# Kernel tuning notes

Hardware: AMD Instinct MI355X
Metric: run time of the kernel (lower is better)

## Reference

```python
import jax, jax.numpy as jnp
import numpy as np

NUM_HEADS = 2
LN_EPS = 1e-5


def layer_norm(x, w, b):
    mu = jnp.mean(x, axis=-1, keepdims=True)
    var = jnp.mean(jnp.square(x - mu), axis=-1, keepdims=True)
    return (x - mu) * jax.lax.rsqrt(var + LN_EPS) * w + b


def setup_inputs() -> dict:
    key = jax.random.key(0)
    ks = jax.random.split(key, 8)
    B, N, C = 8, 2048, 1024
    H = 2 * C  # mlp hidden
    s = lambda fan_in: 1.0 / np.sqrt(fan_in)
    return {
        "x": jax.random.normal(ks[0], (B, N, C), dtype=jnp.float32),
        "ln1_w": jnp.ones((C,), jnp.float32),
        "ln1_b": jnp.zeros((C,), jnp.float32),
        "qkv_w": jax.random.normal(ks[1], (C, 3 * C), jnp.float32) * s(C),
        "qkv_b": jnp.zeros((3 * C,), jnp.float32),
        "proj_w": jax.random.normal(ks[2], (C, C), jnp.float32) * s(C),
        "proj_b": jnp.zeros((C,), jnp.float32),
        "ln2_w": jnp.ones((C,), jnp.float32),
        "ln2_b": jnp.zeros((C,), jnp.float32),
        "mlp_w1": jax.random.normal(ks[3], (C, H), jnp.float32) * s(C),
        "mlp_b1": jnp.zeros((H,), jnp.float32),
        "mlp_w2": jax.random.normal(ks[4], (H, C), jnp.float32) * s(H),
        "mlp_b2": jnp.zeros((C,), jnp.float32),
    }


def reference(x, ln1_w, ln1_b, qkv_w, qkv_b, proj_w, proj_b, ln2_w, ln2_b,
              mlp_w1, mlp_b1, mlp_w2, mlp_b2):
    B, N, C = x.shape
    h = NUM_HEADS
    d = C // h
    scale = d ** -0.5

    # --- attention branch ---
    xn = layer_norm(x, ln1_w, ln1_b)
    qkv = (xn @ qkv_w + qkv_b).reshape(B, N, 3, h, d)
    q, k, v = jnp.moveaxis(qkv, 2, 0)          # each [B, N, h, d]
    q = jnp.swapaxes(q, 1, 2)                  # [B, h, N, d]
    k = jnp.swapaxes(k, 1, 2)
    v = jnp.swapaxes(v, 1, 2)
    attn = jnp.einsum("bhnd,bhmd->bhnm", q, k) * scale
    attn = jax.nn.softmax(attn, axis=-1)       # [B, h, N, N]
    out = jnp.einsum("bhnm,bhmd->bhnd", attn, v)
    out = jnp.swapaxes(out, 1, 2).reshape(B, N, C)
    out = out @ proj_w + proj_b
    x = x + out

    # --- mlp branch ---
    xn = layer_norm(x, ln2_w, ln2_b)
    hdn = jax.nn.gelu(xn @ mlp_w1 + mlp_b1, approximate=False)
    x = x + (hdn @ mlp_w2 + mlp_b2)
    return x
```

## Files before the change

### kernel.cpp

```cpp
#include <hip/hip_runtime.h>
#include <hip/hip_bf16.h>
#include <math.h>

#define TILE 128
#define BK 32

using short8  = __attribute__((ext_vector_type(8))) short;
using short4v = __attribute__((ext_vector_type(4))) short;
using f32x4   = __attribute__((ext_vector_type(4))) float;
typedef __hip_bfloat16 bf16;

constexpr int BB = 8, SEQ = 2048, C = 1024, H3 = 3072, DH = 512, MH = 2048;
constexpr int MR = BB * SEQ;

enum {
  F_TRANSB = 1,
  F_GELU   = 2,
  F_RES    = 4,
  F_OUTBF16= 8,
  F_BIAS   = 16,
  F_SCALE  = 32,
  F_RESF32 = 64
};

struct ZOffs { long long a[16]; long long b[16]; long long c[16]; };

__device__ __forceinline__ float bf2f(bf16 h) { return __bfloat162float(h); }

__device__ __forceinline__ void gload16(const void* g, void* l) {
  __builtin_amdgcn_global_load_lds(
      (const __attribute__((address_space(1))) unsigned int*)g,
      (__attribute__((address_space(3))) unsigned int*)l, 16, 0, 0);
}

template<int FLAGS>
__global__ __launch_bounds__(256) void gemm_k(
    const bf16* __restrict__ A,
    const bf16* __restrict__ B,
    void* __restrict__ Dst,
    const float* __restrict__ bias,
    const void* __restrict__ res,
    int K, int lda, int ldb, int ldc,
    float scale, ZOffs zo)
{
  __shared__ __align__(16) unsigned short As[TILE * BK];
  __shared__ __align__(16) unsigned short Bs[TILE * BK];
  const int tid = threadIdx.x;
  const int z = blockIdx.z;
  const int m0 = blockIdx.y * TILE, n0 = blockIdx.x * TILE;
  const bf16* Ab = A + zo.a[z];
  const bf16* Bb = B + zo.b[z];
  const long long coff = zo.c[z];
  const int wave = tid >> 6, lane = tid & 63;
  const int wm = (wave & 1) << 6, wn = (wave >> 1) << 6;
  const int lr = lane & 15, lq = lane >> 4;

  int srow[2], skb[2];
  #pragma unroll
  for (int i = 0; i < 2; i++) {
    int c = tid + (i << 8);
    srow[i] = c >> 2;
    skb[i]  = (c & 3) ^ ((srow[i] >> 1) & 3);
  }
  const bf16* Asrc[2]; const bf16* Bsrc[2] = {nullptr, nullptr};
  #pragma unroll
  for (int i = 0; i < 2; i++)
    Asrc[i] = Ab + (size_t)(m0 + srow[i]) * lda + skb[i] * 8;
  if (FLAGS & F_TRANSB) {
    #pragma unroll
    for (int i = 0; i < 2; i++)
      Bsrc[i] = Bb + (size_t)(n0 + srow[i]) * ldb + skb[i] * 8;
  }

  f32x4 acc[4][4] = {};
  const int swl = (lr >> 1) & 3;

  for (int k0 = 0; k0 < K; k0 += BK) {
    #pragma unroll
    for (int i = 0; i < 2; i++)
      gload16(Asrc[i] + k0, &As[(tid + (i << 8)) * 8]);
    if (FLAGS & F_TRANSB) {
      #pragma unroll
      for (int i = 0; i < 2; i++)
        gload16(Bsrc[i] + k0, &Bs[(tid + (i << 8)) * 8]);
    } else {
      #pragma unroll
      for (int i = 0; i < 2; i++) {
        int c = tid + (i << 8);
        int kk = c >> 4, nn = (c & 15) << 3;
        unsigned short tmp[8];
        *(uint4*)tmp = *(const uint4*)(Bb + (size_t)(k0 + kk) * ldb + n0 + nn);
        #pragma unroll
        for (int j = 0; j < 8; j++) {
          int n = nn + j;
          Bs[n * BK + (((kk >> 3) ^ ((n >> 1) & 3)) << 3) + (kk & 7)] = tmp[j];
        }
      }
    }
    __syncthreads();
    short8 af[4], bfr[4];
    #pragma unroll
    for (int mi = 0; mi < 4; mi++)
      af[mi] = *(const short8*)&As[(wm + mi * 16 + lr) * BK + ((lq ^ swl) << 3)];
    #pragma unroll
    for (int ni = 0; ni < 4; ni++)
      bfr[ni] = *(const short8*)&Bs[(wn + ni * 16 + lr) * BK + ((lq ^ swl) << 3)];
    #pragma unroll
    for (int mi = 0; mi < 4; mi++)
      #pragma unroll
      for (int ni = 0; ni < 4; ni++)
        acc[mi][ni] = __builtin_amdgcn_mfma_f32_16x16x32_bf16(
            af[mi], bfr[ni], acc[mi][ni], 0, 0, 0);
    __syncthreads();
  }

  #pragma unroll
  for (int mi = 0; mi < 4; mi++) {
    #pragma unroll
    for (int ni = 0; ni < 4; ni++) {
      int col = n0 + wn + ni * 16 + lr;
      float bv = (FLAGS & F_BIAS) ? bias[col] : 0.0f;
      #pragma unroll
      for (int r = 0; r < 4; r++) {
        int row = m0 + wm + mi * 16 + lq * 4 + r;
        float v = acc[mi][ni][r];
        if (FLAGS & F_SCALE) v *= scale;
        v += bv;
        if (FLAGS & F_GELU) v = 0.5f * v * (1.0f + erff(v * 0.70710678118654752f));
        if (FLAGS & F_RES) {
          size_t ridx = (size_t)row * ldc + col;
          v += (FLAGS & F_RESF32) ? ((const float*)res)[ridx]
                                  : bf2f(((const bf16*)res)[ridx]);
        }
        size_t idx = (size_t)coff + (size_t)row * ldc + col;
        if (FLAGS & F_OUTBF16) ((bf16*)Dst)[idx] = __float2bfloat16(v);
        else                   ((float*)Dst)[idx] = v;
      }
    }
  }
}

template<int FLAGS>
__global__ __launch_bounds__(512, 2) void gemm256_k(
    const bf16* __restrict__ A,
    const bf16* __restrict__ B,
    void* __restrict__ Dst,
    const float* __restrict__ bias,
    const void* __restrict__ res,
    int K, int lda, int ldb, int ldc,
    float scale, ZOffs zo)
{
  static_assert(FLAGS & F_TRANSB, "gemm256_k requires B^T layout");
  extern __shared__ __align__(16) unsigned short smem[];
  unsigned short* AsAll = smem;
  unsigned short* BsAll = smem + 4 * 256 * 32;

  const int tid = threadIdx.x;
  const int z = blockIdx.z;
  const int m0 = blockIdx.y * 256, n0 = blockIdx.x * 256;
  const bf16* Ab = A + zo.a[z];
  const bf16* Bb = B + zo.b[z];
  const long long coff = zo.c[z];
  const int wave = tid >> 6, lane = tid & 63;
  const int wm = wave >> 2, wn = wave & 3;
  const int lr = lane & 15, lq = lane >> 4;
  const int swl = (lr >> 1) & 3;
  const int kcol = (lq ^ swl) << 3;

  const bf16* Asrc[2]; const bf16* Bsrc[2];
  #pragma unroll
  for (int i = 0; i < 2; i++) {
    int c = tid + (i << 9);
    int row = c >> 2;
    int ks  = (c & 3) ^ ((row >> 1) & 3);
    Asrc[i] = Ab + (size_t)(m0 + row) * lda + ks * 8;
    Bsrc[i] = Bb + (size_t)(n0 + row) * ldb + ks * 8;
  }
  const int d0 = tid * 8, d1 = (tid + 512) * 8;

  const int nt = K >> 5;

  const int npro = nt < 3 ? nt : 3;
  for (int t = 0; t < npro; ++t) {
    unsigned short* At_ = AsAll + (t & 3) * 8192;
    unsigned short* Bt_ = BsAll + (t & 3) * 8192;
    const int k0 = t * 32;
    gload16(Asrc[0] + k0, At_ + d0);
    gload16(Asrc[1] + k0, At_ + d1);
    gload16(Bsrc[0] + k0, Bt_ + d0);
    gload16(Bsrc[1] + k0, Bt_ + d1);
  }

  f32x4 acc[8][4] = {};
  short8 af[4], bfr[2];

#define RD_A(mh_)                                                            \
  _Pragma("unroll")                                                          \
  for (int m_ = 0; m_ < 4; ++m_)                                             \
    af[m_] = *(const short8*)&At[(wm * 128 + (mh_) * 64 + m_ * 16 + lr) * 32 + kcol];

#define RD_B(nh_)                                                            \
  _Pragma("unroll")                                                          \
  for (int n_ = 0; n_ < 2; ++n_)                                             \
    bfr[n_] = *(const short8*)&Bt[(wn * 64 + (nh_) * 32 + n_ * 16 + lr) * 32 + kcol];

#define MM(mh_, nh_)                                                         \
  __builtin_amdgcn_s_setprio(1);                                             \
  _Pragma("unroll")                                                          \
  for (int m_ = 0; m_ < 4; ++m_)                                             \
    _Pragma("unroll")                                                        \
    for (int n_ = 0; n_ < 2; ++n_)                                           \
      acc[(mh_) * 4 + m_][(nh_) * 2 + n_] =                                  \
          __builtin_amdgcn_mfma_f32_16x16x32_bf16(                           \
              af[m_], bfr[n_], acc[(mh_) * 4 + m_][(nh_) * 2 + n_], 0, 0, 0);\
  __builtin_amdgcn_s_setprio(0);

  for (int t = 0; t < nt; ++t) {
    const int ahead = nt - 1 - t;
    if (ahead >= 2)      asm volatile("s_waitcnt vmcnt(8)" ::: "memory");
    else if (ahead == 1) asm volatile("s_waitcnt vmcnt(4)" ::: "memory");
    else                 asm volatile("s_waitcnt vmcnt(0)" ::: "memory");
    __builtin_amdgcn_s_barrier();

    const unsigned short* At = AsAll + (t & 3) * 8192;
    const unsigned short* Bt = BsAll + (t & 3) * 8192;
    const int ts = t + 3;
    const bool st = ts < nt;
    unsigned short* Ad = AsAll + (ts & 3) * 8192;
    unsigned short* Bd = BsAll + (ts & 3) * 8192;
    const int ks0 = ts * 32;

    RD_A(0); RD_B(0);
    if (st) gload16(Asrc[0] + ks0, Ad + d0);
    __builtin_amdgcn_s_barrier();
    MM(0, 0);
    __builtin_amdgcn_s_barrier();

    RD_B(1);
    if (st) gload16(Asrc[1] + ks0, Ad + d1);
    __builtin_amdgcn_s_barrier();
    MM(0, 1);
    __builtin_amdgcn_s_barrier();

    RD_A(1);
    if (st) gload16(Bsrc[0] + ks0, Bd + d0);
    __builtin_amdgcn_s_barrier();
    MM(1, 1);
    __builtin_amdgcn_s_barrier();

    RD_B(0);
    if (st) gload16(Bsrc[1] + ks0, Bd + d1);
    __builtin_amdgcn_s_barrier();
    MM(1, 0);
    __builtin_amdgcn_s_barrier();
  }

#undef RD_A
#undef RD_B
#undef MM

  const int colBase = n0 + wn * 64 + lr;
  float bv[4];
  #pragma unroll
  for (int n = 0; n < 4; ++n)
    bv[n] = (FLAGS & F_BIAS) ? bias[colBase + n * 16] : 0.0f;
  #pragma unroll
  for (int m = 0; m < 8; ++m) {
    #pragma unroll
    for (int n = 0; n < 4; ++n) {
      const int col = colBase + n * 16;
      #pragma unroll
      for (int r = 0; r < 4; ++r) {
        const int row = m0 + wm * 128 + m * 16 + lq * 4 + r;
        float v = acc[m][n][r];
        if (FLAGS & F_SCALE) v *= scale;
        v += bv[n];
        if (FLAGS & F_GELU) v = 0.5f * v * (1.0f + erff(v * 0.70710678118654752f));
        if (FLAGS & F_RES) {
          size_t ridx = (size_t)row * ldc + col;
          v += (FLAGS & F_RESF32) ? ((const float*)res)[ridx]
                                  : bf2f(((const bf16*)res)[ridx]);
        }
        size_t idx = (size_t)coff + (size_t)row * ldc + col;
        if (FLAGS & F_OUTBF16) ((bf16*)Dst)[idx] = __float2bfloat16(v);
        else                   ((float*)Dst)[idx] = v;
      }
    }
  }
}

__global__ __launch_bounds__(256) void tconv_kernel(
    const float* __restrict__ src, bf16* __restrict__ dst, int K, int N)
{
  __shared__ float t[32][33];
  int n0 = blockIdx.x * 32, k0 = blockIdx.y * 32;
  int c = threadIdx.x & 31, r = threadIdx.x >> 5;
  #pragma unroll
  for (int i = 0; i < 4; i++)
    t[r + i * 8][c] = src[(size_t)(k0 + r + i * 8) * N + n0 + c];
  __syncthreads();
  #pragma unroll
  for (int i = 0; i < 4; i++)
    dst[(size_t)(n0 + r + i * 8) * K + k0 + c] = __float2bfloat16(t[c][r + i * 8]);
}

__global__ __launch_bounds__(256) void vtrans_kernel(
    const bf16* __restrict__ qkv, bf16* __restrict__ vt)
{
  __shared__ unsigned short t[32][33];
  int bh = blockIdx.z, b = bh >> 1, h = bh & 1;
  int n0 = blockIdx.x * 32, d0 = blockIdx.y * 32;
  int c = threadIdx.x & 31, r = threadIdx.x >> 5;
  const bf16* src = qkv + (size_t)b * SEQ * H3 + 2 * C + (size_t)h * DH;
  #pragma unroll
  for (int i = 0; i < 4; i++)
    t[r + i * 8][c] = *(const unsigned short*)&src[(size_t)(n0 + r + i * 8) * H3 + d0 + c];
  __syncthreads();
  bf16* dst = vt + ((size_t)bh * DH + d0) * SEQ + n0;
  #pragma unroll
  for (int i = 0; i < 4; i++)
    *(unsigned short*)&dst[(size_t)(r + i * 8) * SEQ + c] = t[c][r + i * 8];
}

__device__ __forceinline__ void ld4(const float* p, float v[4]) {
  const float4 t = *(const float4*)p;
  v[0] = t.x; v[1] = t.y; v[2] = t.z; v[3] = t.w;
}
__device__ __forceinline__ void ld4(const bf16* p, float v[4]) {
  short4v t = *(const short4v*)p;
  #pragma unroll
  for (int i = 0; i < 4; ++i) v[i] = bf2f(((const bf16*)&t)[i]);
}

template<typename T>
__global__ __launch_bounds__(256) void ln_kernel(
    const T* __restrict__ x,
    const float* __restrict__ w,
    const float* __restrict__ b,
    bf16* __restrict__ out)
{
  __shared__ float sm[4], sm2[4];
  int row = blockIdx.x, tid = threadIdx.x;
  float v[4];
  ld4(x + (size_t)row * 1024 + tid * 4, v);
  float s  = v[0] + v[1] + v[2] + v[3];
  float sq = v[0]*v[0] + v[1]*v[1] + v[2]*v[2] + v[3]*v[3];
  #pragma unroll
  for (int o = 32; o > 0; o >>= 1) {
    s  += __shfl_down(s, o, 64);
    sq += __shfl_down(sq, o, 64);
  }
  int wvi = tid >> 6, lnn = tid & 63;
  if (lnn == 0) { sm[wvi] = s; sm2[wvi] = sq; }
  __syncthreads();
  s  = sm[0] + sm[1] + sm[2] + sm[3];
  sq = sm2[0] + sm2[1] + sm2[2] + sm2[3];
  float mean = s * (1.0f / 1024.0f);
  float var  = sq * (1.0f / 1024.0f) - mean * mean;
  float rs = rsqrtf(var + 1e-5f);
  float wv4[4], bv4[4];
  ld4(w + tid * 4, wv4);
  ld4(b + tid * 4, bv4);
  short4v o4;
  #pragma unroll
  for (int i = 0; i < 4; ++i)
    ((bf16*)&o4)[i] = __float2bfloat16((v[i] - mean) * rs * wv4[i] + bv4[i]);
  *(short4v*)&out[(size_t)row * 1024 + tid * 4] = o4;
}

__global__ __launch_bounds__(256) void softmax_kernel(
    bf16* __restrict__ sc)
{
  __shared__ float sm[4];
  int tid = threadIdx.x;
  size_t base = ((size_t)blockIdx.y * 2048 + blockIdx.x) * 2048 + (size_t)tid * 8;
  short8 sv = *(const short8*)&sc[base];
  float v[8], m = -1e30f;
  #pragma unroll
  for (int i = 0; i < 8; i++) { v[i] = bf2f(((const bf16*)&sv)[i]); m = fmaxf(m, v[i]); }
  #pragma unroll
  for (int o = 32; o > 0; o >>= 1) m = fmaxf(m, __shfl_down(m, o, 64));
  int wvi = tid >> 6, lnn = tid & 63;
  if (lnn == 0) sm[wvi] = m;
  __syncthreads();
  m = fmaxf(fmaxf(sm[0], sm[1]), fmaxf(sm[2], sm[3]));
  __syncthreads();
  float s = 0.f;
  #pragma unroll
  for (int i = 0; i < 8; i++) { v[i] = __expf(v[i] - m); s += v[i]; }
  #pragma unroll
  for (int o = 32; o > 0; o >>= 1) s += __shfl_down(s, o, 64);
  if (lnn == 0) sm[wvi] = s;
  __syncthreads();
  s = sm[0] + sm[1] + sm[2] + sm[3];
  float inv = 1.0f / s;
  short8 ov;
  #pragma unroll
  for (int i = 0; i < 8; i++)
    ((bf16*)&ov)[i] = __float2bfloat16(v[i] * inv);
  *(short8*)&sc[base] = ov;
}

#define G256(FL, grid_, A_, B_, D_, bias_, res_, K_, lda_, ldb_, ldc_, sc_, zo_)      \
  do {                                                                                \
    (void)hipFuncSetAttribute(reinterpret_cast<const void*>(&gemm256_k<(FL)>),        \
                              hipFuncAttributeMaxDynamicSharedMemorySize, 131072);    \
    hipLaunchKernelGGL((gemm256_k<(FL)>), grid_, dim3(512), 131072, stream,           \
                       A_, B_, D_, bias_, res_, K_, lda_, ldb_, ldc_, sc_, zo_);      \
  } while (0)

extern "C" void kernel_launch(void* const* d_in, const int* in_sizes, int n_in,
                              void* d_out, int out_size, void* d_ws, size_t ws_size,
                              hipStream_t stream) {
  const float* x      = (const float*)d_in[0];
  const float* ln1_w  = (const float*)d_in[1];
  const float* ln1_b  = (const float*)d_in[2];
  const float* qkv_w  = (const float*)d_in[3];
  const float* qkv_b  = (const float*)d_in[4];
  const float* proj_w = (const float*)d_in[5];
  const float* proj_b = (const float*)d_in[6];
  const float* ln2_w  = (const float*)d_in[7];
  const float* ln2_b  = (const float*)d_in[8];
  const float* mlp_w1 = (const float*)d_in[9];
  const float* mlp_b1 = (const float*)d_in[10];
  const float* mlp_w2 = (const float*)d_in[11];
  const float* mlp_b2 = (const float*)d_in[12];
  float* out = (float*)d_out;

  char* ws = (char*)d_ws;
  const size_t MB = 1ull << 20;
  bf16* qkvT  = (bf16*)ws;
  bf16* projT = qkvT + 3 * 1024 * 1024;
  bf16* w1T   = qkvT + 4 * 1024 * 1024;
  bf16* w2T   = qkvT + 6 * 1024 * 1024;
  bf16* xn    = (bf16*)(ws + 16 * MB);
  bf16* qkvb  = (bf16*)(ws + 48 * MB);
  bf16* h1    = qkvb;
  bf16* Vt    = (bf16*)(ws + 144 * MB);

  int CH; bool useVt, x1f32;
  if      (ws_size >= 304 * MB) { CH = 16; useVt = true;  x1f32 = true;  }
  else if (ws_size >= 240 * MB) { CH = 8;  useVt = true;  x1f32 = true;  }
  else if (ws_size >= 208 * MB) { CH = 4;  useVt = true;  x1f32 = false; }
  else                          { CH = 4;  useVt = false; x1f32 = false; }
  char* R = ws + (useVt ? 176 * MB : 144 * MB);
  bf16*  scores = (bf16*)R;
  float* x1f    = (float*)R;
  bf16*  x1h    = (bf16*)R;

  ZOffs z0 = {};
  const float scale = 0.04419417382415922f;
  dim3 blk(256);

  hipLaunchKernelGGL(tconv_kernel, dim3(H3 / 32, C / 32), blk, 0, stream, qkv_w, qkvT, C, H3);
  hipLaunchKernelGGL(tconv_kernel, dim3(C / 32, C / 32), blk, 0, stream, proj_w, projT, C, C);
  hipLaunchKernelGGL(tconv_kernel, dim3(MH / 32, C / 32), blk, 0, stream, mlp_w1, w1T, C, MH);
  hipLaunchKernelGGL(tconv_kernel, dim3(C / 32, MH / 32), blk, 0, stream, mlp_w2, w2T, MH, C);

  hipLaunchKernelGGL((ln_kernel<float>), dim3(MR), blk, 0, stream, x, ln1_w, ln1_b, xn);

  G256(F_TRANSB | F_BIAS | F_OUTBF16, dim3(H3 / 256, MR / 256, 1),
       xn, qkvT, (void*)qkvb, qkv_b, nullptr, C, C, C, H3, 1.0f, z0);

  if (useVt)
    hipLaunchKernelGGL(vtrans_kernel, dim3(SEQ / 32, DH / 32, 16), blk, 0, stream, qkvb, Vt);

  for (int ch = 0; ch < 16 / CH; ch++) {
    ZOffs zq = {}, zp = {};
    for (int zz = 0; zz < CH; zz++) {
      int bh = ch * CH + zz, b = bh >> 1, hh = bh & 1;
      zq.a[zz] = (long long)b * SEQ * H3 + (long long)hh * DH;
      zq.b[zz] = (long long)b * SEQ * H3 + C + (long long)hh * DH;
      zq.c[zz] = (long long)zz * SEQ * SEQ;
      zp.a[zz] = (long long)zz * SEQ * SEQ;
      zp.b[zz] = useVt ? (long long)bh * DH * SEQ
                       : (long long)b * SEQ * H3 + 2 * C + (long long)hh * DH;
      zp.c[zz] = (long long)b * SEQ * C + (long long)hh * DH;
    }
    G256(F_TRANSB | F_SCALE | F_OUTBF16, dim3(SEQ / 256, SEQ / 256, CH),
         qkvb, qkvb, (void*)scores, nullptr, nullptr, DH, H3, H3, SEQ, scale, zq);
    hipLaunchKernelGGL(softmax_kernel, dim3(SEQ, CH), blk, 0, stream, scores);
    if (useVt)
      G256(F_TRANSB | F_OUTBF16, dim3(DH / 256, SEQ / 256, CH),
           scores, Vt, (void*)xn, nullptr, nullptr, SEQ, SEQ, SEQ, C, 1.0f, zp);
    else
      hipLaunchKernelGGL((gemm_k<F_OUTBF16>),
                         dim3(DH / TILE, SEQ / TILE, CH), blk, 0, stream,
                         scores, qkvb, (void*)xn, nullptr, nullptr, SEQ, SEQ, H3, C, 1.0f, zp);
  }

  if (x1f32) {
    G256(F_TRANSB | F_BIAS | F_RES | F_RESF32, dim3(C / 256, MR / 256, 1),
         xn, projT, (void*)x1f, proj_b, (const void*)x, C, C, C, C, 1.0f, z0);
    hipLaunchKernelGGL((ln_kernel<float>), dim3(MR), blk, 0, stream, x1f, ln2_w, ln2_b, xn);
  } else {
    G256(F_TRANSB | F_BIAS | F_RES | F_RESF32 | F_OUTBF16, dim3(C / 256, MR / 256, 1),
         xn, projT, (void*)x1h, proj_b, (const void*)x, C, C, C, C, 1.0f, z0);
    hipLaunchKernelGGL((ln_kernel<bf16>), dim3(MR), blk, 0, stream, x1h, ln2_w, ln2_b, xn);
  }

  G256(F_TRANSB | F_BIAS | F_GELU | F_OUTBF16, dim3(MH / 256, MR / 256, 1),
       xn, w1T, (void*)h1, mlp_b1, nullptr, C, C, C, MH, 1.0f, z0);

  if (x1f32) {
    G256(F_TRANSB | F_BIAS | F_RES | F_RESF32, dim3(C / 256, MR / 256, 1),
         h1, w2T, (void*)out, mlp_b2, (const void*)x1f, MH, MH, MH, C, 1.0f, z0);
  } else {
    G256(F_TRANSB | F_BIAS | F_RES, dim3(C / 256, MR / 256, 1),
         h1, w2T, (void*)out, mlp_b2, (const void*)x1h, MH, MH, MH, C, 1.0f, z0);
  }
}
```

Measured before the change: 836.3 us.

## Restructure 256x256 GEMM to BK=64 double buffering with register-held B fragments

The 256-tile GEMM moves from a 4-stage BK=32 LDS ring to a 2-stage BK=64 double buffer with an 8-way XOR swizzle. Each wave keeps both halves of its B fragments in registers so the last MFMA quadrant needs no LDS read, which allows stores into the current buffer during compute and removes one barrier pair per k-step. It also remaps workgroup IDs in groups of eight to improve L2 locality. The cost is more VGPRs for fragments and a shallower prefetch depth in tiles, and the remap assumes the workgroup count divides evenly by eight.

```diff
diff --git a/kernel.cpp b/kernel.cpp
--- a/kernel.cpp
+++ b/kernel.cpp
@@ -152,111 +152,134 @@
 {
   static_assert(FLAGS & F_TRANSB, "gemm256_k requires B^T layout");
   extern __shared__ __align__(16) unsigned short smem[];
-  unsigned short* AsAll = smem;
-  unsigned short* BsAll = smem + 4 * 256 * 32;
 
   const int tid = threadIdx.x;
   const int z = blockIdx.z;
-  const int m0 = blockIdx.y * 256, n0 = blockIdx.x * 256;
+
+  const int gx = gridDim.x;
+  const int nwg = gx * gridDim.y;
+  const int wg = blockIdx.y * gx + blockIdx.x;
+  const int cpx = nwg >> 3;
+  const int swz = (wg & 7) * cpx + (wg >> 3);
+  const int m0 = (swz / gx) * 256, n0 = (swz % gx) * 256;
+
   const bf16* Ab = A + zo.a[z];
   const bf16* Bb = B + zo.b[z];
   const long long coff = zo.c[z];
   const int wave = tid >> 6, lane = tid & 63;
   const int wm = wave >> 2, wn = wave & 3;
   const int lr = lane & 15, lq = lane >> 4;
-  const int swl = (lr >> 1) & 3;
-  const int kcol = (lq ^ swl) << 3;
-
-  const bf16* Asrc[2]; const bf16* Bsrc[2];
-  #pragma unroll
-  for (int i = 0; i < 2; i++) {
-    int c = tid + (i << 9);
-    int row = c >> 2;
-    int ks  = (c & 3) ^ ((row >> 1) & 3);
-    Asrc[i] = Ab + (size_t)(m0 + row) * lda + ks * 8;
-    Bsrc[i] = Bb + (size_t)(n0 + row) * ldb + ks * 8;
-  }
-  const int d0 = tid * 8, d1 = (tid + 512) * 8;
-
-  const int nt = K >> 5;
-
-  const int npro = nt < 3 ? nt : 3;
-  for (int t = 0; t < npro; ++t) {
-    unsigned short* At_ = AsAll + (t & 3) * 8192;
-    unsigned short* Bt_ = BsAll + (t & 3) * 8192;
-    const int k0 = t * 32;
-    gload16(Asrc[0] + k0, At_ + d0);
-    gload16(Asrc[1] + k0, At_ + d1);
-    gload16(Bsrc[0] + k0, Bt_ + d0);
-    gload16(Bsrc[1] + k0, Bt_ + d1);
+  const int r7 = lr & 7;
+  const int sk0 = (lq ^ r7) << 3;
+  const int sk1 = ((4 + lq) ^ r7) << 3;
+  const int rowA = (wm * 128 + lr) * 64;
+  const int rowB = (wn * 64 + lr) * 64;
+
+  const int t8 = tid >> 3, s8 = tid & 7;
+  const int sslot = (s8 ^ (t8 & 7)) << 3;
+  const bf16* srcA = Ab + (size_t)(m0 + t8) * lda + sslot;
+  const int rB0 = (t8 & 31) + ((t8 >> 5) << 6);
+  const bf16* srcB = Bb + (size_t)(n0 + rB0) * ldb + sslot;
+  const int dA0 = tid * 8;
+  const int dB0 = rB0 * 64 + s8 * 8;
+
+  const int nt = K >> 6;
+
+#define SA(h_, ks_, Ad_)                                                       \
+  do {                                                                         \
+    gload16(srcA + (size_t)((h_) * 64) * lda + (ks_),                          \
+            (Ad_) + dA0 + (h_) * 4096);                                        \
+    gload16(srcA + (size_t)((h_) * 64 + 128) * lda + (ks_),                    \
+            (Ad_) + dA0 + (h_) * 4096 + 8192);                                 \
+  } while (0)
+#define SB(h_, ks_, Bd_)                                                       \
+  do {                                                                         \
+    gload16(srcB + (size_t)((h_) * 32) * ldb + (ks_),                          \
+            (Bd_) + dB0 + (h_) * 2048);                                        \
+    gload16(srcB + (size_t)((h_) * 32 + 128) * ldb + (ks_),                    \
+            (Bd_) + dB0 + (h_) * 2048 + 8192);                                 \
+  } while (0)
+
+  {
+    const int npro = nt < 2 ? nt : 2;
+    for (int t = 0; t < npro; ++t) {
+      unsigned short* Ad = smem + (t & 1) * 16384;
+      unsigned short* Bd = smem + 32768 + (t & 1) * 16384;
+      const int ks = t * 64;
+      SA(0, ks, Ad); SA(1, ks, Ad); SB(0, ks, Bd); SB(1, ks, Bd);
+    }
   }
 
   f32x4 acc[8][4] = {};
-  short8 af[4], bfr[2];
-
-#define RD_A(mh_)                                                            \
-  _Pragma("unroll")                                                          \
-  for (int m_ = 0; m_ < 4; ++m_)                                             \
-    af[m_] = *(const short8*)&At[(wm * 128 + (mh_) * 64 + m_ * 16 + lr) * 32 + kcol];
-
-#define RD_B(nh_)                                                            \
-  _Pragma("unroll")                                                          \
-  for (int n_ = 0; n_ < 2; ++n_)                                             \
-    bfr[n_] = *(const short8*)&Bt[(wn * 64 + (nh_) * 32 + n_ * 16 + lr) * 32 + kcol];
-
-#define MM(mh_, nh_)                                                         \
-  __builtin_amdgcn_s_setprio(1);                                             \
-  _Pragma("unroll")                                                          \
-  for (int m_ = 0; m_ < 4; ++m_)                                             \
-    _Pragma("unroll")                                                        \
-    for (int n_ = 0; n_ < 2; ++n_)                                           \
-      acc[(mh_) * 4 + m_][(nh_) * 2 + n_] =                                  \
-          __builtin_amdgcn_mfma_f32_16x16x32_bf16(                           \
-              af[m_], bfr[n_], acc[(mh_) * 4 + m_][(nh_) * 2 + n_], 0, 0, 0);\
+  short8 af0[4], af1[4];
+  short8 bA0[2], bA1[2];
+  short8 bB0[2], bB1[2];
+
+#define RD_AF(mh_)                                                             \
+  _Pragma("unroll")                                                            \
+  for (int m_ = 0; m_ < 4; ++m_) {                                             \
+    af0[m_] = *(const short8*)&At[rowA + ((mh_) * 64 + m_ * 16) * 64 + sk0];   \
+    af1[m_] = *(const short8*)&At[rowA + ((mh_) * 64 + m_ * 16) * 64 + sk1];   \
+  }
+#define RD_BF(nh_, b0_, b1_)                                                   \
+  _Pragma("unroll")                                                            \
+  for (int n_ = 0; n_ < 2; ++n_) {                                             \
+    b0_[n_] = *(const short8*)&Bt[rowB + ((nh_) * 32 + n_ * 16) * 64 + sk0];   \
+    b1_[n_] = *(const short8*)&Bt[rowB + ((nh_) * 32 + n_ * 16) * 64 + sk1];   \
+  }
+#define MM(mh_, nh_, b0_, b1_)                                                 \
+  __builtin_amdgcn_s_setprio(1);                                               \
+  _Pragma("unroll")                                                            \
+  for (int m_ = 0; m_ < 4; ++m_)                                               \
+    _Pragma("unroll")                                                          \
+    for (int n_ = 0; n_ < 2; ++n_) {                                           \
+      acc[(mh_) * 4 + m_][(nh_) * 2 + n_] =                                    \
+          __builtin_amdgcn_mfma_f32_16x16x32_bf16(                             \
+              af0[m_], b0_[n_], acc[(mh_) * 4 + m_][(nh_) * 2 + n_], 0, 0, 0); \
+      acc[(mh_) * 4 + m_][(nh_) * 2 + n_] =                                    \
+          __builtin_amdgcn_mfma_f32_16x16x32_bf16(                             \
+              af1[m_], b1_[n_], acc[(mh_) * 4 + m_][(nh_) * 2 + n_], 0, 0, 0); \
+    }                                                                          \
   __builtin_amdgcn_s_setprio(0);
 
   for (int t = 0; t < nt; ++t) {
-    const int ahead = nt - 1 - t;
-    if (ahead >= 2)      asm volatile("s_waitcnt vmcnt(8)" ::: "memory");
-    else if (ahead == 1) asm volatile("s_waitcnt vmcnt(4)" ::: "memory");
-    else                 asm volatile("s_waitcnt vmcnt(0)" ::: "memory");
-    __builtin_amdgcn_s_barrier();
-
-    const unsigned short* At = AsAll + (t & 3) * 8192;
-    const unsigned short* Bt = BsAll + (t & 3) * 8192;
-    const int ts = t + 3;
-    const bool st = ts < nt;
-    unsigned short* Ad = AsAll + (ts & 3) * 8192;
-    unsigned short* Bd = BsAll + (ts & 3) * 8192;
-    const int ks0 = ts * 32;
-
-    RD_A(0); RD_B(0);
-    if (st) gload16(Asrc[0] + ks0, Ad + d0);
-    __builtin_amdgcn_s_barrier();
-    MM(0, 0);
-    __builtin_amdgcn_s_barrier();
-
-    RD_B(1);
-    if (st) gload16(Asrc[1] + ks0, Ad + d1);
-    __builtin_amdgcn_s_barrier();
-    MM(0, 1);
-    __builtin_amdgcn_s_barrier();
-
-    RD_A(1);
-    if (st) gload16(Bsrc[0] + ks0, Bd + d0);
-    __builtin_amdgcn_s_barrier();
-    MM(1, 1);
-    __builtin_amdgcn_s_barrier();
-
-    RD_B(0);
-    if (st) gload16(Bsrc[1] + ks0, Bd + d1);
-    __builtin_amdgcn_s_barrier();
-    MM(1, 0);
-    __builtin_amdgcn_s_barrier();
-  }
-
-#undef RD_A
-#undef RD_B
+    if (t == nt - 1) asm volatile("s_waitcnt vmcnt(0)" ::: "memory");
+    else             asm volatile("s_waitcnt vmcnt(8)" ::: "memory");
+    __builtin_amdgcn_s_barrier();
+
+    const unsigned short* At = smem + (t & 1) * 16384;
+    const unsigned short* Bt = smem + 32768 + (t & 1) * 16384;
+    unsigned short* Ad = smem + (t & 1) * 16384;
+    unsigned short* Bd = smem + 32768 + (t & 1) * 16384;
+    const bool st = (t + 2) < nt;
+    const int ks = (t + 2) * 64;
+
+    RD_AF(0);
+    RD_BF(0, bA0, bA1);
+    __builtin_amdgcn_s_barrier();
+    MM(0, 0, bA0, bA1);
+    __builtin_amdgcn_s_barrier();
+
+    RD_BF(1, bB0, bB1);
+    if (st) { SA(0, ks, Ad); SB(0, ks, Bd); }
+    __builtin_amdgcn_s_barrier();
+    MM(0, 1, bB0, bB1);
+    __builtin_amdgcn_s_barrier();
+
+    RD_AF(1);
+    if (st) { SB(1, ks, Bd); }
+    __builtin_amdgcn_s_barrier();
+    MM(1, 1, bB0, bB1);
+    __builtin_amdgcn_s_barrier();
+
+    if (st) { SA(1, ks, Ad); }
+    MM(1, 0, bA0, bA1);
+  }
+
+#undef SA
+#undef SB
+#undef RD_AF
+#undef RD_BF
 #undef MM
 
   const int colBase = n0 + wn * 64 + lr;
```

Result: faster. 765.5 us (-8.5%).

## Restructure 256-tile GEMM into 3-stage pipeline with one barrier per K-step and XCD swizzle

Applied to the files above, without the earlier changes.

Replaces the 4-stage LDS ring, which interleaved loads, MFMA phases and eight barriers per K-step, with a 3-stage ring. Each K-step now waits once, issues the global-to-LDS load two steps ahead, and runs all 32 MFMAs after a single barrier. A and B tiles of each stage are packed contiguously, which cuts dynamic LDS from 128 KB to 96 KB. Block indices are also remapped so consecutive workgroups spread across the 8 XCDs in contiguous chunks, to improve L2 reuse. The goal is less barrier overhead and better cache locality, at the cost of one fewer stage of prefetch depth; the swizzle assumes the x*y grid size is divisible by 8.

```diff
diff --git a/kernel.cpp b/kernel.cpp
--- a/kernel.cpp
+++ b/kernel.cpp
@@ -152,12 +152,17 @@
 {
   static_assert(FLAGS & F_TRANSB, "gemm256_k requires B^T layout");
   extern __shared__ __align__(16) unsigned short smem[];
-  unsigned short* AsAll = smem;
-  unsigned short* BsAll = smem + 4 * 256 * 32;
 
   const int tid = threadIdx.x;
   const int z = blockIdx.z;
-  const int m0 = blockIdx.y * 256, n0 = blockIdx.x * 256;
+
+  const int gx = gridDim.x;
+  const int nwg = gx * gridDim.y;
+  const int wg = blockIdx.y * gx + blockIdx.x;
+  const int cpx = nwg >> 3;
+  const int swz = (wg & 7) * cpx + (wg >> 3);
+  const int m0 = (swz / gx) * 256, n0 = (swz % gx) * 256;
+
   const bf16* Ab = A + zo.a[z];
   const bf16* Bb = B + zo.b[z];
   const long long coff = zo.c[z];
@@ -167,97 +172,65 @@
   const int swl = (lr >> 1) & 3;
   const int kcol = (lq ^ swl) << 3;
 
-  const bf16* Asrc[2]; const bf16* Bsrc[2];
-  #pragma unroll
-  for (int i = 0; i < 2; i++) {
-    int c = tid + (i << 9);
-    int row = c >> 2;
-    int ks  = (c & 3) ^ ((row >> 1) & 3);
-    Asrc[i] = Ab + (size_t)(m0 + row) * lda + ks * 8;
-    Bsrc[i] = Bb + (size_t)(n0 + row) * ldb + ks * 8;
-  }
-  const int d0 = tid * 8, d1 = (tid + 512) * 8;
+  const int c0 = tid, c1 = tid + 512;
+  const int row0 = c0 >> 2, sl0 = (c0 & 3) ^ ((row0 >> 1) & 3);
+  const int row1 = c1 >> 2, sl1 = (c1 & 3) ^ ((row1 >> 1) & 3);
+  const bf16* sA0 = Ab + (size_t)(m0 + row0) * lda + sl0 * 8;
+  const bf16* sA1 = Ab + (size_t)(m0 + row1) * lda + sl1 * 8;
+  const bf16* sB0 = Bb + (size_t)(n0 + row0) * ldb + sl0 * 8;
+  const bf16* sB1 = Bb + (size_t)(n0 + row1) * ldb + sl1 * 8;
+  const int dst0 = c0 * 8, dst1 = c1 * 8;
 
   const int nt = K >> 5;
 
-  const int npro = nt < 3 ? nt : 3;
-  for (int t = 0; t < npro; ++t) {
-    unsigned short* At_ = AsAll + (t & 3) * 8192;
-    unsigned short* Bt_ = BsAll + (t & 3) * 8192;
-    const int k0 = t * 32;
-    gload16(Asrc[0] + k0, At_ + d0);
-    gload16(Asrc[1] + k0, At_ + d1);
-    gload16(Bsrc[0] + k0, Bt_ + d0);
-    gload16(Bsrc[1] + k0, Bt_ + d1);
-  }
+#define STAGE(ks_, D_)                                                         \
+  do {                                                                         \
+    gload16(sA0 + (ks_), (D_) + dst0);                                         \
+    gload16(sA1 + (ks_), (D_) + dst1);                                         \
+    gload16(sB0 + (ks_), (D_) + 8192 + dst0);                                  \
+    gload16(sB1 + (ks_), (D_) + 8192 + dst1);                                  \
+  } while (0)
+
+  STAGE(0, smem);
+  if (nt > 1) STAGE(32, smem + 16384);
 
   f32x4 acc[8][4] = {};
-  short8 af[4], bfr[2];
-
-#define RD_A(mh_)                                                            \
-  _Pragma("unroll")                                                          \
-  for (int m_ = 0; m_ < 4; ++m_)                                             \
-    af[m_] = *(const short8*)&At[(wm * 128 + (mh_) * 64 + m_ * 16 + lr) * 32 + kcol];
-
-#define RD_B(nh_)                                                            \
-  _Pragma("unroll")                                                          \
-  for (int n_ = 0; n_ < 2; ++n_)                                             \
-    bfr[n_] = *(const short8*)&Bt[(wn * 64 + (nh_) * 32 + n_ * 16 + lr) * 32 + kcol];
-
-#define MM(mh_, nh_)                                                         \
-  __builtin_amdgcn_s_setprio(1);                                             \
-  _Pragma("unroll")                                                          \
-  for (int m_ = 0; m_ < 4; ++m_)                                             \
-    _Pragma("unroll")                                                        \
-    for (int n_ = 0; n_ < 2; ++n_)                                           \
-      acc[(mh_) * 4 + m_][(nh_) * 2 + n_] =                                  \
-          __builtin_amdgcn_mfma_f32_16x16x32_bf16(                           \
-              af[m_], bfr[n_], acc[(mh_) * 4 + m_][(nh_) * 2 + n_], 0, 0, 0);\
-  __builtin_amdgcn_s_setprio(0);
+  short8 af[4], bf4[4];
+  int bc = 0, bs = 2;
 
   for (int t = 0; t < nt; ++t) {
-    const int ahead = nt - 1 - t;
-    if (ahead >= 2)      asm volatile("s_waitcnt vmcnt(8)" ::: "memory");
-    else if (ahead == 1) asm volatile("s_waitcnt vmcnt(4)" ::: "memory");
-    else                 asm volatile("s_waitcnt vmcnt(0)" ::: "memory");
+    if (t == nt - 1) asm volatile("s_waitcnt vmcnt(0)" ::: "memory");
+    else             asm volatile("s_waitcnt vmcnt(4)" ::: "memory");
     __builtin_amdgcn_s_barrier();
-
-    const unsigned short* At = AsAll + (t & 3) * 8192;
-    const unsigned short* Bt = BsAll + (t & 3) * 8192;
-    const int ts = t + 3;
-    const bool st = ts < nt;
-    unsigned short* Ad = AsAll + (ts & 3) * 8192;
-    unsigned short* Bd = BsAll + (ts & 3) * 8192;
-    const int ks0 = ts * 32;
-
-    RD_A(0); RD_B(0);
-    if (st) gload16(Asrc[0] + ks0, Ad + d0);
-    __builtin_amdgcn_s_barrier();
-    MM(0, 0);
-    __builtin_amdgcn_s_barrier();
-
-    RD_B(1);
-    if (st) gload16(Asrc[1] + ks0, Ad + d1);
-    __builtin_amdgcn_s_barrier();
-    MM(0, 1);
-    __builtin_amdgcn_s_barrier();
-
-    RD_A(1);
-    if (st) gload16(Bsrc[0] + ks0, Bd + d0);
-    __builtin_amdgcn_s_barrier();
-    MM(1, 1);
-    __builtin_amdgcn_s_barrier();
-
-    RD_B(0);
-    if (st) gload16(Bsrc[1] + ks0, Bd + d1);
-    __builtin_amdgcn_s_barrier();
-    MM(1, 0);
-    __builtin_amdgcn_s_barrier();
-  }
-
-#undef RD_A
-#undef RD_B
-#undef MM
+    asm volatile("" ::: "memory");
+
+    if (t + 2 < nt) STAGE((t + 2) * 32, smem + bs * 16384);
+
+    const unsigned short* At = smem + bc * 16384;
+    const unsigned short* Bt = At + 8192;
+
+    #pragma unroll
+    for (int n_ = 0; n_ < 4; ++n_)
+      bf4[n_] = *(const short8*)&Bt[(wn * 64 + n_ * 16 + lr) * 32 + kcol];
+    #pragma unroll
+    for (int mh = 0; mh < 2; ++mh) {
+      #pragma unroll
+      for (int m_ = 0; m_ < 4; ++m_)
+        af[m_] = *(const short8*)&At[(wm * 128 + mh * 64 + m_ * 16 + lr) * 32 + kcol];
+      __builtin_amdgcn_s_setprio(1);
+      #pragma unroll
+      for (int m_ = 0; m_ < 4; ++m_)
+        #pragma unroll
+        for (int n_ = 0; n_ < 4; ++n_)
+          acc[mh * 4 + m_][n_] = __builtin_amdgcn_mfma_f32_16x16x32_bf16(
+              af[m_], bf4[n_], acc[mh * 4 + m_][n_], 0, 0, 0);
+      __builtin_amdgcn_s_setprio(0);
+    }
+    bc = bc == 2 ? 0 : bc + 1;
+    bs = bs == 2 ? 0 : bs + 1;
+  }
+
+#undef STAGE
 
   const int colBase = n0 + wn * 64 + lr;
   float bv[4];
@@ -404,8 +377,8 @@
 #define G256(FL, grid_, A_, B_, D_, bias_, res_, K_, lda_, ldb_, ldc_, sc_, zo_)      \
   do {                                                                                \
     (void)hipFuncSetAttribute(reinterpret_cast<const void*>(&gemm256_k<(FL)>),        \
-                              hipFuncAttributeMaxDynamicSharedMemorySize, 131072);    \
-    hipLaunchKernelGGL((gemm256_k<(FL)>), grid_, dim3(512), 131072, stream,           \
+                              hipFuncAttributeMaxDynamicSharedMemorySize, 98304);     \
+    hipLaunchKernelGGL((gemm256_k<(FL)>), grid_, dim3(512), 98304, stream,            \
                        A_, B_, D_, bias_, res_, K_, lda_, ldb_, ldc_, sc_, zo_);      \
   } while (0)
 
```

New measurement: 801.9 us. 4.1% less time.
